# Optimization experiments

Measured on AMD Instinct MI355X. Metric: run time of the kernel, lower is better.

## Reference

```python
import jax, jax.numpy as jnp
import numpy as np

BN_EPS = 1e-5


def _gin_layer(x, src, dst, Wa, ba, Wb, bb, n_nodes):
    # GINConv (eps=0): h_i = MLP(x_i + sum_{j in N(i)} x_j)
    agg = jax.ops.segment_sum(x[src], dst, num_segments=n_nodes)
    h = x + agg
    h = jnp.maximum(h @ Wa + ba, 0.0) @ Wb + bb
    return h


def _bn(x, g, b, m, v):
    return (x - m) * jax.lax.rsqrt(v + BN_EPS) * g + b


def setup_inputs() -> dict:
    key = jax.random.key(0)
    ks = jax.random.split(key, 32)
    N, F, D, C, E = 50000, 128, 32, 10, 800000
    inp = {
        "x": jax.random.normal(ks[0], (N, F), dtype=jnp.float32),
        "edge_index": jax.random.randint(ks[1], (2, E), 0, N, dtype=jnp.int32),
    }
    def lin(k, fi, fo):
        s = 1.0 / np.sqrt(fi)
        kw, kb = jax.random.split(k)
        return (jax.random.uniform(kw, (fi, fo), jnp.float32, -s, s),
                jax.random.uniform(kb, (fo,), jnp.float32, -s, s))
    inp["W1a"], inp["b1a"] = lin(ks[2], F, D)
    inp["W1b"], inp["b1b"] = lin(ks[3], D, D)
    inp["W2a"], inp["b2a"] = lin(ks[4], D, D)
    inp["W2b"], inp["b2b"] = lin(ks[5], D, D)
    inp["W3a"], inp["b3a"] = lin(ks[6], D, D)
    inp["W3b"], inp["b3b"] = lin(ks[7], D, D)
    for i in (1, 2, 3):
        inp[f"g{i}"] = jnp.ones((D,), jnp.float32)
        inp[f"be{i}"] = jnp.zeros((D,), jnp.float32)
        inp[f"m{i}"] = jax.random.normal(ks[8 + i], (D,), jnp.float32) * 0.1
        inp[f"v{i}"] = jax.random.uniform(ks[12 + i], (D,), jnp.float32, 0.5, 1.5)
    inp["Wf1"], inp["bf1"] = lin(ks[20], D, D)
    inp["Wf2"], inp["bf2"] = lin(ks[21], D, C)
    return inp


def reference(x, edge_index,
              W1a, b1a, W1b, b1b, W2a, b2a, W2b, b2b, W3a, b3a, W3b, b3b,
              g1, be1, m1, v1, g2, be2, m2, v2, g3, be3, m3, v3,
              Wf1, bf1, Wf2, bf2):
    n = x.shape[0]
    src, dst = edge_index[0], edge_index[1]
    h = jnp.maximum(_gin_layer(x, src, dst, W1a, b1a, W1b, b1b, n), 0.0)
    h = _bn(h, g1, be1, m1, v1)
    h = jnp.maximum(_gin_layer(h, src, dst, W2a, b2a, W2b, b2b, n), 0.0)
    h = _bn(h, g2, be2, m2, v2)
    h = jnp.maximum(_gin_layer(h, src, dst, W3a, b3a, W3b, b3b, n), 0.0)
    h = _bn(h, g3, be3, m3, v3)
    h = jnp.maximum(h @ Wf1 + bf1, 0.0)
    # dropout is identity in inference mode
    h = h @ Wf2 + bf2
    return jax.nn.log_softmax(h, axis=-1)
```

## Files before the change

### kernel.cpp

```cpp
#include <hip/hip_runtime.h>

#define BN_EPS 1e-5f
#define PART_STRIPES 160
#define CAP 64

__device__ inline float4 bf4_to_f4(ushort4 u) {
    float4 f;
    f.x = __uint_as_float((unsigned)u.x << 16);
    f.y = __uint_as_float((unsigned)u.y << 16);
    f.z = __uint_as_float((unsigned)u.z << 16);
    f.w = __uint_as_float((unsigned)u.w << 16);
    return f;
}
__device__ inline ushort f_to_bf(float f) {
    unsigned b = __float_as_uint(f);
    return (ushort)((b + 0x7FFFu + ((b >> 16) & 1u)) >> 16);
}
__device__ inline ushort4 f4_to_bf4(float4 f) {
    ushort4 u;
    u.x = f_to_bf(f.x); u.y = f_to_bf(f.y); u.z = f_to_bf(f.z); u.w = f_to_bf(f.w);
    return u;
}

__global__ void zero_ints(int* __restrict__ p, int n4) {
    int i = blockIdx.x * blockDim.x + threadIdx.x;
    if (i < n4) reinterpret_cast<int4*>(p)[i] = make_int4(0, 0, 0, 0);
}

__global__ void place_and_gemm(const int* __restrict__ src, const int* __restrict__ dst,
                               int* __restrict__ cursor, int* __restrict__ ssrc,
                               int E, int n,
                               const float* __restrict__ x, const float* __restrict__ W,
                               ushort* __restrict__ z, int placeBlocks) {
    __shared__ __align__(16) float sW[128 * 32];
    __shared__ __align__(16) float sIn[32][132];
    int b = blockIdx.x;
    if (b < placeBlocks) {
        int g = b & 7;
        int sb = b >> 3;
        int rstep = (n + 7) / 8;
        int lo = g * rstep;
        int hi = lo + rstep; if (hi > n) hi = n;
        int per = (E + PART_STRIPES - 1) / PART_STRIPES;
        int e0 = sb * per;
        int e1 = e0 + per; if (e1 > E) e1 = E;

        auto doedge = [&](int d, int s) {
            if (d >= lo && d < hi) {
                int k = atomicAdd(&cursor[d], 1);
                if (k < CAP) ssrc[((size_t)d << 6) + k] = s;
            }
        };
        for (int base = e0 + threadIdx.x * 4; base < e1; base += 1024) {
            if (base + 3 < e1) {
                const int4 d4 = *reinterpret_cast<const int4*>(dst + base);
                const int4 s4 = *reinterpret_cast<const int4*>(src + base);
                doedge(d4.x, s4.x);
                doedge(d4.y, s4.y);
                doedge(d4.z, s4.z);
                doedge(d4.w, s4.w);
            } else {
                int stop = base + 4; if (stop > e1) stop = e1;
                for (int e = base; e < stop; e++) doedge(dst[e], src[e]);
            }
        }
        return;
    }

    int blk = b - placeBlocks;
    int tid = threadIdx.x;
    for (int i = tid; i < 128 * 32; i += 256) sW[i] = W[i];
    {
        int base = blk * 32;
        #pragma unroll
        for (int q = 0; q < 4; q++) {
            int flat = tid * 4 + q * 1024;
            int r = flat >> 7, cc = flat & 127;
            int node = base + r;
            float4 xv = make_float4(0.f, 0.f, 0.f, 0.f);
            if (node < n) xv = *reinterpret_cast<const float4*>(x + (size_t)node * 128 + cc);
            *reinterpret_cast<float4*>(&sIn[r][cc]) = xv;
        }
    }
    __syncthreads();

    int grp = tid >> 3, lane = tid & 7, c = lane * 4;
    int node = blk * 32 + grp;
    float4 acc = make_float4(0.f, 0.f, 0.f, 0.f);
    #pragma unroll 8
    for (int k4 = 0; k4 < 32; k4++) {
        const float4 t4 = *reinterpret_cast<const float4*>(&sIn[grp][k4 * 4]);
        #pragma unroll
        for (int kk = 0; kk < 4; kk++) {
            float tk = (kk == 0) ? t4.x : (kk == 1) ? t4.y : (kk == 2) ? t4.z : t4.w;
            const float4 w = *reinterpret_cast<const float4*>(&sW[(k4 * 4 + kk) * 32 + c]);
            acc.x += tk * w.x; acc.y += tk * w.y; acc.z += tk * w.z; acc.w += tk * w.w;
        }
    }
    if (node < n) *reinterpret_cast<ushort4*>(z + (size_t)node * 32 + c) = f4_to_bf4(acc);
}

#define GATHER_BODY(zptr)                                                        \
    int j = j0;                                                                  \
    for (; j + 7 < j1; j += 8) {                                                 \
        int idxv = ssrc[j + lane];                                               \
        int s0 = __shfl(idxv, 0, 8); int s1 = __shfl(idxv, 1, 8);                \
        int s2 = __shfl(idxv, 2, 8); int s3 = __shfl(idxv, 3, 8);                \
        int s4 = __shfl(idxv, 4, 8); int s5 = __shfl(idxv, 5, 8);                \
        int s6 = __shfl(idxv, 6, 8); int s7 = __shfl(idxv, 7, 8);                \
        float4 v0 = bf4_to_f4(*reinterpret_cast<const ushort4*>(zptr + (size_t)s0 * 32 + c)); \
        float4 v1 = bf4_to_f4(*reinterpret_cast<const ushort4*>(zptr + (size_t)s1 * 32 + c)); \
        float4 v2 = bf4_to_f4(*reinterpret_cast<const ushort4*>(zptr + (size_t)s2 * 32 + c)); \
        float4 v3 = bf4_to_f4(*reinterpret_cast<const ushort4*>(zptr + (size_t)s3 * 32 + c)); \
        float4 v4 = bf4_to_f4(*reinterpret_cast<const ushort4*>(zptr + (size_t)s4 * 32 + c)); \
        float4 v5 = bf4_to_f4(*reinterpret_cast<const ushort4*>(zptr + (size_t)s5 * 32 + c)); \
        float4 v6 = bf4_to_f4(*reinterpret_cast<const ushort4*>(zptr + (size_t)s6 * 32 + c)); \
        float4 v7 = bf4_to_f4(*reinterpret_cast<const ushort4*>(zptr + (size_t)s7 * 32 + c)); \
        acc.x += (v0.x + v1.x) + (v2.x + v3.x);                                  \
        acc.y += (v0.y + v1.y) + (v2.y + v3.y);                                  \
        acc.z += (v0.z + v1.z) + (v2.z + v3.z);                                  \
        acc.w += (v0.w + v1.w) + (v2.w + v3.w);                                  \
        acc2.x += (v4.x + v5.x) + (v6.x + v7.x);                                 \
        acc2.y += (v4.y + v5.y) + (v6.y + v7.y);                                 \
        acc2.z += (v4.z + v5.z) + (v6.z + v7.z);                                 \
        acc2.w += (v4.w + v5.w) + (v6.w + v7.w);                                 \
    }                                                                            \
    for (; j + 1 < j1; j += 2) {                                                 \
        int s0 = ssrc[j];     int s1 = ssrc[j + 1];                              \
        float4 v0 = bf4_to_f4(*reinterpret_cast<const ushort4*>(zptr + (size_t)s0 * 32 + c)); \
        float4 v1 = bf4_to_f4(*reinterpret_cast<const ushort4*>(zptr + (size_t)s1 * 32 + c)); \
        acc.x += v0.x + v1.x; acc.y += v0.y + v1.y;                              \
        acc.z += v0.z + v1.z; acc.w += v0.w + v1.w;                              \
    }                                                                            \
    if (j < j1) {                                                                \
        int s0 = ssrc[j];                                                        \
        float4 v0 = bf4_to_f4(*reinterpret_cast<const ushort4*>(zptr + (size_t)s0 * 32 + c)); \
        acc.x += v0.x; acc.y += v0.y; acc.z += v0.z; acc.w += v0.w;              \
    }                                                                            \
    acc.x += acc2.x; acc.y += acc2.y; acc.z += acc2.z; acc.w += acc2.w;

#define MATMUL32(sWx, hv)                                                        \
    _Pragma("unroll")                                                            \
    for (int k4 = 0; k4 < 8; k4++) {                                             \
        const float4 t4 = *reinterpret_cast<const float4*>(&sT[grp][k4 * 4]);    \
        const float4 wa = *reinterpret_cast<const float4*>(&sWx[(k4 * 4 + 0) * 32 + c]); \
        const float4 wb = *reinterpret_cast<const float4*>(&sWx[(k4 * 4 + 1) * 32 + c]); \
        const float4 wc = *reinterpret_cast<const float4*>(&sWx[(k4 * 4 + 2) * 32 + c]); \
        const float4 wd = *reinterpret_cast<const float4*>(&sWx[(k4 * 4 + 3) * 32 + c]); \
        hv.x += t4.x * wa.x + t4.y * wb.x + t4.z * wc.x + t4.w * wd.x;           \
        hv.y += t4.x * wa.y + t4.y * wb.y + t4.z * wc.y + t4.w * wd.y;           \
        hv.z += t4.x * wa.z + t4.y * wb.z + t4.z * wc.z + t4.w * wd.z;           \
        hv.w += t4.x * wa.w + t4.y * wb.w + t4.z * wc.w + t4.w * wd.w;           \
    }

__global__ void gin_fused_mid(const ushort* __restrict__ z, const int* __restrict__ cnt,
                              const int* __restrict__ ssrc,
                              const float* __restrict__ ba, const float* __restrict__ Wb,
                              const float* __restrict__ bb,
                              const float* __restrict__ g, const float* __restrict__ be,
                              const float* __restrict__ m, const float* __restrict__ v,
                              const float* __restrict__ Wn, ushort* __restrict__ zout, int n) {
    __shared__ __align__(16) float sWb[1024];
    __shared__ __align__(16) float sWn[1024];
    __shared__ __align__(16) float sT[32][36];
    int tid = threadIdx.x;
    for (int i = tid; i < 1024; i += 256) { sWb[i] = Wb[i]; sWn[i] = Wn[i]; }
    int grp = tid >> 3, lane = tid & 7, c = lane * 4;
    int node = blockIdx.x * 32 + grp;

    float4 acc = make_float4(0.f, 0.f, 0.f, 0.f);
    float4 acc2 = make_float4(0.f, 0.f, 0.f, 0.f);
    int j0 = 0, j1 = 0;
    if (node < n) {
        acc = bf4_to_f4(*reinterpret_cast<const ushort4*>(z + (size_t)node * 32 + c));
        int d = cnt[node]; d = d < CAP ? d : CAP;
        j0 = node << 6;
        j1 = j0 + d;
    }
    GATHER_BODY(z)

    const float4 bav = *reinterpret_cast<const float4*>(ba + c);
    sT[grp][c + 0] = fmaxf(acc.x + bav.x, 0.0f);
    sT[grp][c + 1] = fmaxf(acc.y + bav.y, 0.0f);
    sT[grp][c + 2] = fmaxf(acc.z + bav.z, 0.0f);
    sT[grp][c + 3] = fmaxf(acc.w + bav.w, 0.0f);
    __syncthreads();

    float4 h = *reinterpret_cast<const float4*>(bb + c);
    MATMUL32(sWb, h)
    const float4 mv = *reinterpret_cast<const float4*>(m + c);
    const float4 vv = *reinterpret_cast<const float4*>(v + c);
    const float4 gv = *reinterpret_cast<const float4*>(g + c);
    const float4 bev = *reinterpret_cast<const float4*>(be + c);
    float4 o;
    o.x = (fmaxf(h.x, 0.f) - mv.x) * rsqrtf(vv.x + BN_EPS) * gv.x + bev.x;
    o.y = (fmaxf(h.y, 0.f) - mv.y) * rsqrtf(vv.y + BN_EPS) * gv.y + bev.y;
    o.z = (fmaxf(h.z, 0.f) - mv.z) * rsqrtf(vv.z + BN_EPS) * gv.z + bev.z;
    o.w = (fmaxf(h.w, 0.f) - mv.w) * rsqrtf(vv.w + BN_EPS) * gv.w + bev.w;
    __syncthreads();
    sT[grp][c + 0] = o.x;
    sT[grp][c + 1] = o.y;
    sT[grp][c + 2] = o.z;
    sT[grp][c + 3] = o.w;
    __syncthreads();

    float4 zq = make_float4(0.f, 0.f, 0.f, 0.f);
    MATMUL32(sWn, zq)
    if (node < n) *reinterpret_cast<ushort4*>(zout + (size_t)node * 32 + c) = f4_to_bf4(zq);
}

__global__ void gin_fused_last(const ushort* __restrict__ z, const int* __restrict__ cnt,
                               const int* __restrict__ ssrc,
                               const float* __restrict__ ba, const float* __restrict__ Wb,
                               const float* __restrict__ bb,
                               const float* __restrict__ g, const float* __restrict__ be,
                               const float* __restrict__ m, const float* __restrict__ v,
                               const float* __restrict__ Wf1, const float* __restrict__ bf1,
                               const float* __restrict__ Wf2, const float* __restrict__ bf2,
                               float* __restrict__ out, int n) {
    __shared__ __align__(16) float sWb[1024];
    __shared__ __align__(16) float sW1[1024];
    __shared__ float sW2[320];
    __shared__ __align__(16) float sT[32][36];
    __shared__ float sZ[32][12];
    int tid = threadIdx.x;
    for (int i = tid; i < 1024; i += 256) { sWb[i] = Wb[i]; sW1[i] = Wf1[i]; }
    for (int i = tid; i < 320; i += 256) sW2[i] = Wf2[i];
    int grp = tid >> 3, lane = tid & 7, c = lane * 4;
    int node = blockIdx.x * 32 + grp;

    float4 acc = make_float4(0.f, 0.f, 0.f, 0.f);
    float4 acc2 = make_float4(0.f, 0.f, 0.f, 0.f);
    int j0 = 0, j1 = 0;
    if (node < n) {
        acc = bf4_to_f4(*reinterpret_cast<const ushort4*>(z + (size_t)node * 32 + c));
        int d = cnt[node]; d = d < CAP ? d : CAP;
        j0 = node << 6;
        j1 = j0 + d;
    }
    GATHER_BODY(z)

    const float4 bav = *reinterpret_cast<const float4*>(ba + c);
    sT[grp][c + 0] = fmaxf(acc.x + bav.x, 0.0f);
    sT[grp][c + 1] = fmaxf(acc.y + bav.y, 0.0f);
    sT[grp][c + 2] = fmaxf(acc.z + bav.z, 0.0f);
    sT[grp][c + 3] = fmaxf(acc.w + bav.w, 0.0f);
    __syncthreads();

    float4 h = *reinterpret_cast<const float4*>(bb + c);
    MATMUL32(sWb, h)
    const float4 mv = *reinterpret_cast<const float4*>(m + c);
    const float4 vv = *reinterpret_cast<const float4*>(v + c);
    const float4 gv = *reinterpret_cast<const float4*>(g + c);
    const float4 bev = *reinterpret_cast<const float4*>(be + c);
    float4 o;
    o.x = (fmaxf(h.x, 0.f) - mv.x) * rsqrtf(vv.x + BN_EPS) * gv.x + bev.x;
    o.y = (fmaxf(h.y, 0.f) - mv.y) * rsqrtf(vv.y + BN_EPS) * gv.y + bev.y;
    o.z = (fmaxf(h.z, 0.f) - mv.z) * rsqrtf(vv.z + BN_EPS) * gv.z + bev.z;
    o.w = (fmaxf(h.w, 0.f) - mv.w) * rsqrtf(vv.w + BN_EPS) * gv.w + bev.w;
    __syncthreads();
    sT[grp][c + 0] = o.x;
    sT[grp][c + 1] = o.y;
    sT[grp][c + 2] = o.z;
    sT[grp][c + 3] = o.w;
    __syncthreads();

    float4 t2 = *reinterpret_cast<const float4*>(bf1 + c);
    MATMUL32(sW1, t2)
    t2.x = fmaxf(t2.x, 0.f); t2.y = fmaxf(t2.y, 0.f);
    t2.z = fmaxf(t2.z, 0.f); t2.w = fmaxf(t2.w, 0.f);
    __syncthreads();
    sT[grp][c + 0] = t2.x;
    sT[grp][c + 1] = t2.y;
    sT[grp][c + 2] = t2.z;
    sT[grp][c + 3] = t2.w;
    __syncthreads();

    for (int jj = lane; jj < 10; jj += 8) {
        float l = bf2[jj];
        #pragma unroll
        for (int k4 = 0; k4 < 8; k4++) {
            const float4 t4 = *reinterpret_cast<const float4*>(&sT[grp][k4 * 4]);
            l += t4.x * sW2[(k4 * 4 + 0) * 10 + jj];
            l += t4.y * sW2[(k4 * 4 + 1) * 10 + jj];
            l += t4.z * sW2[(k4 * 4 + 2) * 10 + jj];
            l += t4.w * sW2[(k4 * 4 + 3) * 10 + jj];
        }
        sZ[grp][jj] = l;
    }
    __syncthreads();

    if (node < n) {
        float mx = sZ[grp][0];
        #pragma unroll
        for (int jj = 1; jj < 10; jj++) mx = fmaxf(mx, sZ[grp][jj]);
        float s = 0.0f;
        #pragma unroll
        for (int jj = 0; jj < 10; jj++) s += __expf(sZ[grp][jj] - mx);
        float lse = mx + logf(s);
        for (int jj = lane; jj < 10; jj += 8)
            out[(size_t)node * 10 + jj] = sZ[grp][jj] - lse;
    }
}

extern "C" void kernel_launch(void* const* d_in, const int* in_sizes, int n_in,
                              void* d_out, int out_size, void* d_ws, size_t ws_size,
                              hipStream_t stream) {
    const float* x   = (const float*)d_in[0];
    const int*   ei  = (const int*)d_in[1];
    const float* W1a = (const float*)d_in[2];
    const float* b1a = (const float*)d_in[3];
    const float* W1b = (const float*)d_in[4];
    const float* b1b = (const float*)d_in[5];
    const float* W2a = (const float*)d_in[6];
    const float* b2a = (const float*)d_in[7];
    const float* W2b = (const float*)d_in[8];
    const float* b2b = (const float*)d_in[9];
    const float* W3a = (const float*)d_in[10];
    const float* b3a = (const float*)d_in[11];
    const float* W3b = (const float*)d_in[12];
    const float* b3b = (const float*)d_in[13];
    const float* g1  = (const float*)d_in[14];
    const float* be1 = (const float*)d_in[15];
    const float* m1  = (const float*)d_in[16];
    const float* v1  = (const float*)d_in[17];
    const float* g2  = (const float*)d_in[18];
    const float* be2 = (const float*)d_in[19];
    const float* m2  = (const float*)d_in[20];
    const float* v2  = (const float*)d_in[21];
    const float* g3  = (const float*)d_in[22];
    const float* be3 = (const float*)d_in[23];
    const float* m3  = (const float*)d_in[24];
    const float* v3  = (const float*)d_in[25];
    const float* Wf1 = (const float*)d_in[26];
    const float* bf1 = (const float*)d_in[27];
    const float* Wf2 = (const float*)d_in[28];
    const float* bf2 = (const float*)d_in[29];

    const int n = in_sizes[0] / 128;
    const int E = in_sizes[1] / 2;
    const int* src = ei;
    const int* dst = ei + E;

    ushort* zA = (ushort*)d_ws;
    ushort* zB = zA + (size_t)n * 32;
    int* cursor = (int*)(zB + (size_t)n * 32);
    int* ssrc   = cursor + n;

    float* out = (float*)d_out;
    const int nodeBlocks32 = (n + 31) / 32;
    const int placeBlocks = PART_STRIPES * 8;
    const int nz4 = (n + 3) / 4;

    zero_ints<<<(nz4 + 255) / 256, 256, 0, stream>>>(cursor, nz4);
    place_and_gemm<<<placeBlocks + nodeBlocks32, 256, 0, stream>>>(
        src, dst, cursor, ssrc, E, n, x, W1a, zA, placeBlocks);

    gin_fused_mid<<<nodeBlocks32, 256, 0, stream>>>(zA, cursor, ssrc, b1a, W1b, b1b,
                                                    g1, be1, m1, v1, W2a, zB, n);
    gin_fused_mid<<<nodeBlocks32, 256, 0, stream>>>(zB, cursor, ssrc, b2a, W2b, b2b,
                                                    g2, be2, m2, v2, W3a, zA, n);
    gin_fused_last<<<nodeBlocks32, 256, 0, stream>>>(zA, cursor, ssrc, b3a, W3b, b3b,
                                                     g3, be3, m3, v3, Wf1, bf1, Wf2, bf2,
                                                     out, n);
}
```

Measured before the change: 113.1 us.

## Drop range-partitioned edge placement; pad per-node cursors to 64-byte stride

Edge placement no longer has each block scan its stripe of edges eight times, once per destination range. Each thread now handles four edges once and does atomics directly. Per-node counters are padded to a 16-int stride so atomics from different nodes fall on separate cache lines, which should cut contention and false sharing. In exchange the atomics become scattered across a 16x larger counter array, which costs more memory to zero and hurts locality when the counts are read back in the gather kernels.

```diff
diff --git a/kernel.cpp b/kernel.cpp
--- a/kernel.cpp
+++ b/kernel.cpp
@@ -1,8 +1,8 @@
 #include <hip/hip_runtime.h>
 
 #define BN_EPS 1e-5f
-#define PART_STRIPES 160
 #define CAP 64
+#define CSTRIDE 16
 
 __device__ inline float4 bf4_to_f4(ushort4 u) {
     float4 f;
@@ -36,32 +36,24 @@
     __shared__ __align__(16) float sIn[32][132];
     int b = blockIdx.x;
     if (b < placeBlocks) {
-        int g = b & 7;
-        int sb = b >> 3;
-        int rstep = (n + 7) / 8;
-        int lo = g * rstep;
-        int hi = lo + rstep; if (hi > n) hi = n;
-        int per = (E + PART_STRIPES - 1) / PART_STRIPES;
-        int e0 = sb * per;
-        int e1 = e0 + per; if (e1 > E) e1 = E;
-
-        auto doedge = [&](int d, int s) {
-            if (d >= lo && d < hi) {
-                int k = atomicAdd(&cursor[d], 1);
-                if (k < CAP) ssrc[((size_t)d << 6) + k] = s;
-            }
-        };
-        for (int base = e0 + threadIdx.x * 4; base < e1; base += 1024) {
-            if (base + 3 < e1) {
-                const int4 d4 = *reinterpret_cast<const int4*>(dst + base);
-                const int4 s4 = *reinterpret_cast<const int4*>(src + base);
-                doedge(d4.x, s4.x);
-                doedge(d4.y, s4.y);
-                doedge(d4.z, s4.z);
-                doedge(d4.w, s4.w);
-            } else {
-                int stop = base + 4; if (stop > e1) stop = e1;
-                for (int e = base; e < stop; e++) doedge(dst[e], src[e]);
+        int base = (b * 256 + threadIdx.x) * 4;
+        if (base + 3 < E) {
+            const int4 d4 = *reinterpret_cast<const int4*>(dst + base);
+            const int4 s4 = *reinterpret_cast<const int4*>(src + base);
+            int k;
+            k = atomicAdd(&cursor[d4.x * CSTRIDE], 1);
+            if (k < CAP) ssrc[((size_t)d4.x << 6) + k] = s4.x;
+            k = atomicAdd(&cursor[d4.y * CSTRIDE], 1);
+            if (k < CAP) ssrc[((size_t)d4.y << 6) + k] = s4.y;
+            k = atomicAdd(&cursor[d4.z * CSTRIDE], 1);
+            if (k < CAP) ssrc[((size_t)d4.z << 6) + k] = s4.z;
+            k = atomicAdd(&cursor[d4.w * CSTRIDE], 1);
+            if (k < CAP) ssrc[((size_t)d4.w << 6) + k] = s4.w;
+        } else if (base < E) {
+            for (int e = base; e < E; e++) {
+                int d = dst[e];
+                int k = atomicAdd(&cursor[d * CSTRIDE], 1);
+                if (k < CAP) ssrc[((size_t)d << 6) + k] = src[e];
             }
         }
         return;
@@ -71,12 +63,12 @@
     int tid = threadIdx.x;
     for (int i = tid; i < 128 * 32; i += 256) sW[i] = W[i];
     {
-        int base = blk * 32;
+        int nb = blk * 32;
         #pragma unroll
         for (int q = 0; q < 4; q++) {
             int flat = tid * 4 + q * 1024;
             int r = flat >> 7, cc = flat & 127;
-            int node = base + r;
+            int node = nb + r;
             float4 xv = make_float4(0.f, 0.f, 0.f, 0.f);
             if (node < n) xv = *reinterpret_cast<const float4*>(x + (size_t)node * 128 + cc);
             *reinterpret_cast<float4*>(&sIn[r][cc]) = xv;
@@ -173,7 +165,7 @@
     int j0 = 0, j1 = 0;
     if (node < n) {
         acc = bf4_to_f4(*reinterpret_cast<const ushort4*>(z + (size_t)node * 32 + c));
-        int d = cnt[node]; d = d < CAP ? d : CAP;
+        int d = cnt[node * CSTRIDE]; d = d < CAP ? d : CAP;
         j0 = node << 6;
         j1 = j0 + d;
     }
@@ -234,7 +226,7 @@
     int j0 = 0, j1 = 0;
     if (node < n) {
         acc = bf4_to_f4(*reinterpret_cast<const ushort4*>(z + (size_t)node * 32 + c));
-        int d = cnt[node]; d = d < CAP ? d : CAP;
+        int d = cnt[node * CSTRIDE]; d = d < CAP ? d : CAP;
         j0 = node << 6;
         j1 = j0 + d;
     }
@@ -345,12 +337,12 @@
     ushort* zA = (ushort*)d_ws;
     ushort* zB = zA + (size_t)n * 32;
     int* cursor = (int*)(zB + (size_t)n * 32);
-    int* ssrc   = cursor + n;
+    int* ssrc   = cursor + (size_t)n * CSTRIDE;
 
     float* out = (float*)d_out;
     const int nodeBlocks32 = (n + 31) / 32;
-    const int placeBlocks = PART_STRIPES * 8;
-    const int nz4 = (n + 3) / 4;
+    const int placeBlocks = (E / 4 + 255) / 256;
+    const int nz4 = (n * CSTRIDE) / 4;
 
     zero_ints<<<(nz4 + 255) / 256, 256, 0, stream>>>(cursor, nz4);
     place_and_gemm<<<placeBlocks + nodeBlocks32, 256, 0, stream>>>(
```

After: 137.8 us. 21.9% more time.
